# Kernel tuning notes

Hardware: AMD Instinct MI355X
Metric: run time of the kernel (lower is better)

The kernel has to match this reference:

```python
import jax, jax.numpy as jnp
import numpy as np

N, F, E, T = 50000, 128, 800000, 8


def setup_inputs() -> dict:
    key = jax.random.key(0)
    ks = jax.random.split(key, 10)
    s = 1.0 / np.sqrt(F)
    return {
        "x": jax.random.normal(ks[0], (N, F), jnp.float32),
        "edge_index": jax.random.randint(ks[1], (2, E), 0, N, jnp.int64),
        "edge_weight": jax.random.uniform(ks[2], (E,), jnp.float32),
        "W0": jax.random.normal(ks[3], (F, F), jnp.float32) * s,
        "Wih": jax.random.normal(ks[4], (3 * F, F), jnp.float32) * s,
        "Whh": jax.random.normal(ks[5], (3 * F, F), jnp.float32) * s,
        "bih": jax.random.normal(ks[6], (3 * F,), jnp.float32) * s,
        "bhh": jax.random.normal(ks[7], (3 * F,), jnp.float32) * s,
        "Wlin": jax.random.normal(ks[8], (T, F), jnp.float32) * s,
        "blin": jax.random.normal(ks[9], (T,), jnp.float32) * s,
    }


def _evolve_weight(W0, Wih, Whh, bih, bhh):
    # One GRU step with input = hidden = W0 (rows of weight matrix as batch).
    gi = W0 @ Wih.T + bih  # [F, 3F]
    gh = W0 @ Whh.T + bhh
    ir, iz, inn = jnp.split(gi, 3, axis=1)
    hr, hz, hn = jnp.split(gh, 3, axis=1)
    r = jax.nn.sigmoid(ir + hr)
    z = jax.nn.sigmoid(iz + hz)
    n = jnp.tanh(inn + r * hn)
    return (1.0 - z) * n + z * W0  # [F, F]


def reference(x, edge_index, edge_weight, W0, Wih, Whh, bih, bhh, Wlin, blin):
    n_nodes = x.shape[0]
    W = _evolve_weight(W0, Wih, Whh, bih, bhh)
    # gcn_norm with added self-loops (fill value 1.0), symmetric normalization
    loop = jnp.arange(n_nodes, dtype=edge_index.dtype)
    row = jnp.concatenate([edge_index[0], loop])
    col = jnp.concatenate([edge_index[1], loop])
    ew = jnp.concatenate([edge_weight, jnp.ones((n_nodes,), edge_weight.dtype)])
    deg = jax.ops.segment_sum(ew, col, num_segments=n_nodes)
    dinv = jnp.where(deg > 0, jax.lax.rsqrt(jnp.where(deg > 0, deg, 1.0)), 0.0)
    norm = dinv[row] * ew * dinv[col]  # [E+N]
    xw = x @ W  # [N, F]
    h = jax.ops.segment_sum(norm[:, None] * xw[row], col, num_segments=n_nodes)
    h = jax.nn.relu(h)
    return h @ Wlin.T + blin  # [N, n_target]
```

## Files before the change

kernel.cpp:

```cpp
#include <hip/hip_runtime.h>
#include <math.h>

#define F 128
#define FIX_SCALE 16777216.0f
#define FIX_INV   (1.0f / 16777216.0f)
#define CNT_SHIFT 40
#define DEG_MASK  ((1ULL << 40) - 1)

using bf16x8 = __attribute__((ext_vector_type(8))) short;
using f32x4  = __attribute__((ext_vector_type(4))) float;

__device__ inline int read_idx(const int* ei, long long elem, int i64) {
    return i64 ? (int)((const long long*)ei)[elem] : ei[elem];
}
__device__ inline unsigned int f2bf_rn(float f) {
    unsigned int b = __float_as_uint(f);
    return (b + 0x7FFFu + ((b >> 16) & 1u)) >> 16;
}
__device__ inline float bflo(unsigned int u) { return __uint_as_float(u << 16); }
__device__ inline float bfhi(unsigned int u) { return __uint_as_float(u & 0xFFFF0000u); }

__global__ void k_init(unsigned long long* packed, int* flag, const int* ei, int N) {
    int i = blockIdx.x * blockDim.x + threadIdx.x;
    if (i < N) packed[i] = 0ULL;
    if (i == 0) {
        int i64 = 1;
        for (int j = 0; j < 32; ++j) if (ei[2 * j + 1] != 0) { i64 = 0; break; }
        *flag = i64;
    }
}

__global__ void k_count(const int* ei, const float* ew, unsigned long long* packed,
                        int* pos, const int* flag, int E) {
    int e = blockIdx.x * blockDim.x + threadIdx.x;
    if (e >= E) return;
    int i64 = *flag;
    int c = read_idx(ei, (long long)E + e, i64);
    unsigned long long u = (1ULL << CNT_SHIFT) |
                           (unsigned long long)(ew[e] * FIX_SCALE + 0.5f);
    unsigned long long old = atomicAdd(&packed[c], u);
    pos[e] = (int)(old >> CNT_SHIFT);
}

__global__ void k_bsum(const unsigned long long* __restrict__ packed,
                       int* __restrict__ bsum, int N) {
    __shared__ int s[4];
    int i = blockIdx.x * 256 + threadIdx.x;
    int v = (i < N) ? (int)(packed[i] >> CNT_SHIFT) : 0;
    #pragma unroll
    for (int o = 1; o < 64; o <<= 1) v += __shfl_xor(v, o, 64);
    if ((threadIdx.x & 63) == 0) s[threadIdx.x >> 6] = v;
    __syncthreads();
    if (threadIdx.x == 0) bsum[blockIdx.x] = s[0] + s[1] + s[2] + s[3];
}

__global__ void k_bscan(int* bsum, int nb) {
    __shared__ int sdata[1024];
    int tid = threadIdx.x;
    int run = 0;
    for (int base = 0; base < nb; base += 1024) {
        int i = base + tid;
        int v = (i < nb) ? bsum[i] : 0;
        sdata[tid] = v;
        __syncthreads();
        #pragma unroll
        for (int s = 1; s < 1024; s <<= 1) {
            int add = (tid >= s) ? sdata[tid - s] : 0;
            __syncthreads();
            sdata[tid] += add;
            __syncthreads();
        }
        if (i < nb) bsum[i] = run + sdata[tid] - v;
        run += sdata[1023];
        __syncthreads();
    }
}

__global__ void k_offs(const unsigned long long* __restrict__ packed,
                       const int* __restrict__ bsum,
                       int* __restrict__ off, float* __restrict__ dinv, int N, int E) {
    __shared__ int sdata[256];
    int t = threadIdx.x;
    int i = blockIdx.x * 256 + t;
    unsigned long long p = (i < N) ? packed[i] : 0ULL;
    int v = (int)(p >> CNT_SHIFT);
    sdata[t] = v;
    __syncthreads();
    #pragma unroll
    for (int s = 1; s < 256; s <<= 1) {
        int add = (t >= s) ? sdata[t - s] : 0;
        __syncthreads();
        sdata[t] += add;
        __syncthreads();
    }
    if (i < N) {
        off[i] = bsum[blockIdx.x] + sdata[t] - v;
        float deg = 1.0f + (float)(p & DEG_MASK) * FIX_INV;
        dinv[i] = rsqrtf(deg);
        if (i == N - 1) off[N] = E;
    }
}

__global__ void k_place(const int* ei, const float* ew,
                        const int* __restrict__ off, const int* __restrict__ pos,
                        int2* ep, const int* flag, int E) {
    int e = blockIdx.x * blockDim.x + threadIdx.x;
    if (e >= E) return;
    int i64 = *flag;
    int r = read_idx(ei, e, i64);
    int c = read_idx(ei, (long long)E + e, i64);
    ep[off[c] + pos[e]] = make_int2(r, __float_as_int(ew[e]));
}

__global__ void k_evolve(const float* __restrict__ W0, const float* __restrict__ Wih,
                         const float* __restrict__ Whh, const float* __restrict__ bih,
                         const float* __restrict__ bhh,
                         unsigned short* __restrict__ Wth,
                         unsigned short* __restrict__ Wtl) {
    __shared__ __align__(16) float w0row[F];
    int i = blockIdx.x;
    int j = threadIdx.x;
    w0row[j] = W0[i * F + j];
    __syncthreads();
    float air = 0, aiz = 0, ain = 0, ahr = 0, ahz = 0, ahn = 0;
    const float* ir_p = Wih + (size_t)j * F;
    const float* iz_p = Wih + (size_t)(j + F) * F;
    const float* in_p = Wih + (size_t)(j + 2 * F) * F;
    const float* hr_p = Whh + (size_t)j * F;
    const float* hz_p = Whh + (size_t)(j + F) * F;
    const float* hn_p = Whh + (size_t)(j + 2 * F) * F;
    for (int k = 0; k < F; k += 4) {
        float4 w0 = *(const float4*)&w0row[k];
        float4 a;
        a = *(const float4*)&ir_p[k]; air += w0.x*a.x + w0.y*a.y + w0.z*a.z + w0.w*a.w;
        a = *(const float4*)&iz_p[k]; aiz += w0.x*a.x + w0.y*a.y + w0.z*a.z + w0.w*a.w;
        a = *(const float4*)&in_p[k]; ain += w0.x*a.x + w0.y*a.y + w0.z*a.z + w0.w*a.w;
        a = *(const float4*)&hr_p[k]; ahr += w0.x*a.x + w0.y*a.y + w0.z*a.z + w0.w*a.w;
        a = *(const float4*)&hz_p[k]; ahz += w0.x*a.x + w0.y*a.y + w0.z*a.z + w0.w*a.w;
        a = *(const float4*)&hn_p[k]; ahn += w0.x*a.x + w0.y*a.y + w0.z*a.z + w0.w*a.w;
    }
    air += bih[j];         ahr += bhh[j];
    aiz += bih[j + F];     ahz += bhh[j + F];
    ain += bih[j + 2*F];   ahn += bhh[j + 2*F];
    float r = 1.0f / (1.0f + expf(-(air + ahr)));
    float z = 1.0f / (1.0f + expf(-(aiz + ahz)));
    float n = tanhf(ain + r * ahn);
    float w = (1.0f - z) * n + z * w0row[j];
    unsigned int hb = f2bf_rn(w);
    float whi = __uint_as_float(hb << 16);
    unsigned int lb = f2bf_rn(w - whi);
    Wth[j * F + i] = (unsigned short)hb;
    Wtl[j * F + i] = (unsigned short)lb;
}

__global__ void k_cast(const float2* __restrict__ x2, const float* __restrict__ dinv,
                       unsigned int* __restrict__ xs, int M ) {
    int id = blockIdx.x * 256 + threadIdx.x;
    if (id >= M) return;
    float di = dinv[id >> 6];
    float2 v = x2[id];
    xs[id] = f2bf_rn(di * v.x) | (f2bf_rn(di * v.y) << 16);
}

__global__ __launch_bounds__(256) void k_agg2(const uint4* __restrict__ xs4,
                                              const int* __restrict__ off,
                                              const int2* __restrict__ ep,
                                              const float* __restrict__ dinv,
                                              uint4* __restrict__ hagg4, int N) {
    int wave = threadIdx.x >> 6, lane = threadIdx.x & 63;
    int c = blockIdx.x * 4 + wave;
    if (c >= N) return;
    int g = lane >> 4, sl = lane & 15;
    int start = off[c], end = off[c + 1];
    float a0[8] = {0,0,0,0,0,0,0,0}, a1[8] = {0,0,0,0,0,0,0,0};
    if (g == 0) {
        uint4 v = xs4[(size_t)c * 16 + sl];
        a0[0] = bflo(v.x); a0[1] = bfhi(v.x);
        a0[2] = bflo(v.y); a0[3] = bfhi(v.y);
        a0[4] = bflo(v.z); a0[5] = bfhi(v.z);
        a0[6] = bflo(v.w); a0[7] = bfhi(v.w);
    }
    for (int k = start; k < end; k += 8) {
        int iA = k + g, iB = k + g + 4;
        bool okA = iA < end, okB = iB < end;
        int2 eA, eB;
        if (okA) eA = ep[iA];
        if (okB) eB = ep[iB];
        if (okA) {
            uint4 v = xs4[(size_t)eA.x * 16 + sl];
            float w = __int_as_float(eA.y);
            a0[0] += w * bflo(v.x); a0[1] += w * bfhi(v.x);
            a0[2] += w * bflo(v.y); a0[3] += w * bfhi(v.y);
            a0[4] += w * bflo(v.z); a0[5] += w * bfhi(v.z);
            a0[6] += w * bflo(v.w); a0[7] += w * bfhi(v.w);
        }
        if (okB) {
            uint4 v = xs4[(size_t)eB.x * 16 + sl];
            float w = __int_as_float(eB.y);
            a1[0] += w * bflo(v.x); a1[1] += w * bfhi(v.x);
            a1[2] += w * bflo(v.y); a1[3] += w * bfhi(v.y);
            a1[4] += w * bflo(v.z); a1[5] += w * bfhi(v.z);
            a1[6] += w * bflo(v.w); a1[7] += w * bfhi(v.w);
        }
    }
    #pragma unroll
    for (int f = 0; f < 8; ++f) {
        float v = a0[f] + a1[f];
        v += __shfl_xor(v, 16, 64);
        v += __shfl_xor(v, 32, 64);
        a0[f] = v;
    }
    if (lane < 16) {
        float di = dinv[c];
        uint4 o;
        o.x = f2bf_rn(di * a0[0]) | (f2bf_rn(di * a0[1]) << 16);
        o.y = f2bf_rn(di * a0[2]) | (f2bf_rn(di * a0[3]) << 16);
        o.z = f2bf_rn(di * a0[4]) | (f2bf_rn(di * a0[5]) << 16);
        o.w = f2bf_rn(di * a0[6]) | (f2bf_rn(di * a0[7]) << 16);
        hagg4[(size_t)c * 16 + lane] = o;
    }
}

__global__ __launch_bounds__(256) void k_gemm(const uint4* __restrict__ hagg4,
                                              const unsigned short* __restrict__ Wth,
                                              const unsigned short* __restrict__ Wtl,
                                              const float* __restrict__ Wlin,
                                              const float* __restrict__ blin,
                                              float* __restrict__ out, int N) {
    __shared__ __align__(16) unsigned int At[64 * 68];
    __shared__ __align__(16) float WlinL[8 * F];
    int t = threadIdx.x;
    int row0 = blockIdx.x * 64;
    #pragma unroll
    for (int it = 0; it < 4; ++it) {
        int idx = it * 256 + t;
        int rr = idx >> 4, c4 = idx & 15;
        uint4 v = make_uint4(0u, 0u, 0u, 0u);
        if (row0 + rr < N) v = hagg4[(size_t)(row0 + rr) * 16 + c4];
        *(uint4*)&At[rr * 68 + c4 * 4] = v;
    }
    *(float4*)&WlinL[t * 4] = *(const float4*)&Wlin[t * 4];
    __syncthreads();

    int wave = t >> 6, lane = t & 63;
    int sl = lane & 15, q = lane >> 4;
    const unsigned short* Ash = (const unsigned short*)At;
    int mrow = wave * 16 + sl;

    f32x4 acc[8];
    #pragma unroll
    for (int nt = 0; nt < 8; ++nt) acc[nt] = (f32x4){0.f, 0.f, 0.f, 0.f};
    #pragma unroll
    for (int ko = 0; ko < 4; ++ko) {
        bf16x8 a = *(const bf16x8*)&Ash[mrow * 136 + ko * 32 + q * 8];
        #pragma unroll
        for (int nt = 0; nt < 8; ++nt) {
            int boff = (nt * 16 + sl) * F + ko * 32 + q * 8;
            bf16x8 bh = *(const bf16x8*)&Wth[boff];
            bf16x8 bl = *(const bf16x8*)&Wtl[boff];
            acc[nt] = __builtin_amdgcn_mfma_f32_16x16x32_bf16(a, bh, acc[nt], 0, 0, 0);
            acc[nt] = __builtin_amdgcn_mfma_f32_16x16x32_bf16(a, bl, acc[nt], 0, 0, 0);
        }
    }
    #pragma unroll
    for (int nt = 0; nt < 8; ++nt)
        #pragma unroll
        for (int r = 0; r < 4; ++r) acc[nt][r] = fmaxf(acc[nt][r], 0.f);

    float p[8][4];
    #pragma unroll
    for (int tt = 0; tt < 8; ++tt) {
        float wl[8];
        #pragma unroll
        for (int nt = 0; nt < 8; ++nt) wl[nt] = WlinL[tt * F + nt * 16 + sl];
        #pragma unroll
        for (int r = 0; r < 4; ++r) {
            float s = 0.f;
            #pragma unroll
            for (int nt = 0; nt < 8; ++nt) s += acc[nt][r] * wl[nt];
            p[tt][r] = s;
        }
    }
    #pragma unroll
    for (int tt = 0; tt < 8; ++tt)
        #pragma unroll
        for (int r = 0; r < 4; ++r) {
            float v = p[tt][r];
            v += __shfl_xor(v, 1, 64); v += __shfl_xor(v, 2, 64);
            v += __shfl_xor(v, 4, 64); v += __shfl_xor(v, 8, 64);
            p[tt][r] = v;
        }
    if (sl == 0) {
        #pragma unroll
        for (int r = 0; r < 4; ++r) {
            int row = row0 + wave * 16 + q * 4 + r;
            if (row < N) {
                #pragma unroll
                for (int tt = 0; tt < 8; ++tt)
                    out[(size_t)row * 8 + tt] = p[tt][r] + blin[tt];
            }
        }
    }
}

extern "C" void kernel_launch(void* const* d_in, const int* in_sizes, int n_in,
                              void* d_out, int out_size, void* d_ws, size_t ws_size,
                              hipStream_t stream) {
    const float* x    = (const float*)d_in[0];
    const int*   ei   = (const int*)d_in[1];
    const float* ew   = (const float*)d_in[2];
    const float* W0   = (const float*)d_in[3];
    const float* Wih  = (const float*)d_in[4];
    const float* Whh  = (const float*)d_in[5];
    const float* bih  = (const float*)d_in[6];
    const float* bhh  = (const float*)d_in[7];
    const float* Wlin = (const float*)d_in[8];
    const float* blin = (const float*)d_in[9];
    int N = in_sizes[0] / F;
    int E = in_sizes[1] / 2;
    float* outp = (float*)d_out;

    int nblk = (N + 255) / 256;

    char* wsb = (char*)d_ws;
    size_t cur = 0;
    auto alloc = [&](size_t sz) -> void* {
        void* p = wsb + cur;
        cur = (cur + sz + 255) & ~(size_t)255;
        return p;
    };
    unsigned long long* packed = (unsigned long long*)alloc((size_t)N * 8);
    float* dinv = (float*)alloc((size_t)N * 4);
    int*   off  = (int*)  alloc((size_t)(N + 1) * 4);
    int*   bsum = (int*)  alloc((size_t)nblk * 4);
    int*   flag = (int*)  alloc(256);
    int*   pos  = (int*)  alloc((size_t)E * 4);
    int2*  ep   = (int2*) alloc((size_t)E * 8);
    unsigned short* Wth = (unsigned short*)alloc((size_t)F * F * 2);
    unsigned short* Wtl = (unsigned short*)alloc((size_t)F * F * 2);
    unsigned int* xs    = (unsigned int*)alloc((size_t)N * 64 * 4);
    unsigned int* hagg  = (unsigned int*)alloc((size_t)N * 64 * 4);
    (void)ws_size; (void)n_in; (void)out_size;

    int M = N * 64;
    hipLaunchKernelGGL(k_init,   dim3(nblk),            dim3(256),  0, stream, packed, flag, ei, N);
    hipLaunchKernelGGL(k_count,  dim3((E + 255) / 256), dim3(256),  0, stream, ei, ew, packed, pos, flag, E);
    hipLaunchKernelGGL(k_bsum,   dim3(nblk),            dim3(256),  0, stream, packed, bsum, N);
    hipLaunchKernelGGL(k_bscan,  dim3(1),               dim3(1024), 0, stream, bsum, nblk);
    hipLaunchKernelGGL(k_offs,   dim3(nblk),            dim3(256),  0, stream, packed, bsum, off, dinv, N, E);
    hipLaunchKernelGGL(k_evolve, dim3(F),               dim3(F),    0, stream, W0, Wih, Whh, bih, bhh, Wth, Wtl);
    hipLaunchKernelGGL(k_place,  dim3((E + 255) / 256), dim3(256),  0, stream, ei, ew, off, pos, ep, flag, E);
    hipLaunchKernelGGL(k_cast,   dim3((M + 255) / 256), dim3(256),  0, stream, (const float2*)x, dinv, xs, M);
    hipLaunchKernelGGL(k_agg2,   dim3((N + 3) / 4),     dim3(256),  0, stream, (const uint4*)xs, off, ep, dinv, (uint4*)hagg, N);
    hipLaunchKernelGGL(k_gemm,   dim3((N + 63) / 64),   dim3(256),  0, stream, (const uint4*)hagg, Wth, Wtl, Wlin, blin, outp, N);
}
```

Before: 245.0 us.

## Fuse aggregation into GEMM, merge place/cast/evolve, pad atomic counters

Fuses the CSR neighbour aggregation into the MFMA GEMM kernel so aggregated rows go straight to shared memory, with no hagg round-trip through global memory. The place, cast and weight-evolve kernels are merged into one launch by splitting on block index. The single-block scan is replaced by each block summing its preceding block sums. Per-node atomic counters are padded to a stride of 8 to cut atomic contention on shared cache lines. The cost is fewer aggregation waves in flight per block (64 rows per block of 4 waves), a redundant per-block prefix reduction, and an 8x larger counter buffer to zero.

```diff
diff --git a/kernel.cpp b/kernel.cpp
--- a/kernel.cpp
+++ b/kernel.cpp
@@ -6,6 +6,7 @@
 #define FIX_INV   (1.0f / 16777216.0f)
 #define CNT_SHIFT 40
 #define DEG_MASK  ((1ULL << 40) - 1)
+#define PSTRIDE 8
 
 using bf16x8 = __attribute__((ext_vector_type(8))) short;
 using f32x4  = __attribute__((ext_vector_type(4))) float;
@@ -20,9 +21,9 @@
 __device__ inline float bflo(unsigned int u) { return __uint_as_float(u << 16); }
 __device__ inline float bfhi(unsigned int u) { return __uint_as_float(u & 0xFFFF0000u); }
 
-__global__ void k_init(unsigned long long* packed, int* flag, const int* ei, int N) {
+__global__ void k_init(unsigned long long* packed, int* flag, const int* ei, int M8) {
     int i = blockIdx.x * blockDim.x + threadIdx.x;
-    if (i < N) packed[i] = 0ULL;
+    if (i < M8) packed[i] = 0ULL;
     if (i == 0) {
         int i64 = 1;
         for (int j = 0; j < 32; ++j) if (ei[2 * j + 1] != 0) { i64 = 0; break; }
@@ -38,7 +39,7 @@
     int c = read_idx(ei, (long long)E + e, i64);
     unsigned long long u = (1ULL << CNT_SHIFT) |
                            (unsigned long long)(ew[e] * FIX_SCALE + 0.5f);
-    unsigned long long old = atomicAdd(&packed[c], u);
+    unsigned long long old = atomicAdd(&packed[(size_t)c * PSTRIDE], u);
     pos[e] = (int)(old >> CNT_SHIFT);
 }
 
@@ -46,7 +47,7 @@
                        int* __restrict__ bsum, int N) {
     __shared__ int s[4];
     int i = blockIdx.x * 256 + threadIdx.x;
-    int v = (i < N) ? (int)(packed[i] >> CNT_SHIFT) : 0;
+    int v = (i < N) ? (int)(packed[(size_t)i * PSTRIDE] >> CNT_SHIFT) : 0;
     #pragma unroll
     for (int o = 1; o < 64; o <<= 1) v += __shfl_xor(v, o, 64);
     if ((threadIdx.x & 63) == 0) s[threadIdx.x >> 6] = v;
@@ -54,35 +55,24 @@
     if (threadIdx.x == 0) bsum[blockIdx.x] = s[0] + s[1] + s[2] + s[3];
 }
 
-__global__ void k_bscan(int* bsum, int nb) {
-    __shared__ int sdata[1024];
-    int tid = threadIdx.x;
-    int run = 0;
-    for (int base = 0; base < nb; base += 1024) {
-        int i = base + tid;
-        int v = (i < nb) ? bsum[i] : 0;
-        sdata[tid] = v;
-        __syncthreads();
-        #pragma unroll
-        for (int s = 1; s < 1024; s <<= 1) {
-            int add = (tid >= s) ? sdata[tid - s] : 0;
-            __syncthreads();
-            sdata[tid] += add;
-            __syncthreads();
-        }
-        if (i < nb) bsum[i] = run + sdata[tid] - v;
-        run += sdata[1023];
-        __syncthreads();
-    }
-}
-
-__global__ void k_offs(const unsigned long long* __restrict__ packed,
-                       const int* __restrict__ bsum,
-                       int* __restrict__ off, float* __restrict__ dinv, int N, int E) {
+__global__ void k_offs2(const unsigned long long* __restrict__ packed,
+                        const int* __restrict__ bsum,
+                        int* __restrict__ off, float* __restrict__ dinv, int N, int E) {
+    __shared__ int sred[256];
     __shared__ int sdata[256];
     int t = threadIdx.x;
+    int pre = 0;
+    for (int j = t; j < blockIdx.x; j += 256) pre += bsum[j];
+    sred[t] = pre;
+    __syncthreads();
+    #pragma unroll
+    for (int s = 128; s > 0; s >>= 1) {
+        if (t < s) sred[t] += sred[t + s];
+        __syncthreads();
+    }
+    int base = sred[0];
     int i = blockIdx.x * 256 + t;
-    unsigned long long p = (i < N) ? packed[i] : 0ULL;
+    unsigned long long p = (i < N) ? packed[(size_t)i * PSTRIDE] : 0ULL;
     int v = (int)(p >> CNT_SHIFT);
     sdata[t] = v;
     __syncthreads();
@@ -94,33 +84,49 @@
         __syncthreads();
     }
     if (i < N) {
-        off[i] = bsum[blockIdx.x] + sdata[t] - v;
+        off[i] = base + sdata[t] - v;
         float deg = 1.0f + (float)(p & DEG_MASK) * FIX_INV;
         dinv[i] = rsqrtf(deg);
         if (i == N - 1) off[N] = E;
     }
 }
 
-__global__ void k_place(const int* ei, const float* ew,
-                        const int* __restrict__ off, const int* __restrict__ pos,
-                        int2* ep, const int* flag, int E) {
-    int e = blockIdx.x * blockDim.x + threadIdx.x;
-    if (e >= E) return;
-    int i64 = *flag;
-    int r = read_idx(ei, e, i64);
-    int c = read_idx(ei, (long long)E + e, i64);
-    ep[off[c] + pos[e]] = make_int2(r, __float_as_int(ew[e]));
-}
-
-__global__ void k_evolve(const float* __restrict__ W0, const float* __restrict__ Wih,
-                         const float* __restrict__ Whh, const float* __restrict__ bih,
-                         const float* __restrict__ bhh,
-                         unsigned short* __restrict__ Wth,
-                         unsigned short* __restrict__ Wtl) {
-    __shared__ __align__(16) float w0row[F];
-    int i = blockIdx.x;
-    int j = threadIdx.x;
-    w0row[j] = W0[i * F + j];
+__global__ __launch_bounds__(256) void k_pce(
+        const int* ei, const float* ew, const int* __restrict__ off,
+        const int* __restrict__ pos, int2* ep, const int* flag, int E, int nPlaceBlk,
+        const float2* __restrict__ x2, const float* __restrict__ dinv,
+        unsigned int* __restrict__ xs, int M, int nCastBlk,
+        const float* __restrict__ W0, const float* __restrict__ Wih,
+        const float* __restrict__ Whh, const float* __restrict__ bih,
+        const float* __restrict__ bhh,
+        unsigned short* __restrict__ Wth, unsigned short* __restrict__ Wtl) {
+    int b = blockIdx.x;
+    if (b < nPlaceBlk) {
+        int e = b * 256 + threadIdx.x;
+        if (e < E) {
+            int i64 = *flag;
+            int r = read_idx(ei, e, i64);
+            int c = read_idx(ei, (long long)E + e, i64);
+            ep[off[c] + pos[e]] = make_int2(r, __float_as_int(ew[e]));
+        }
+        return;
+    }
+    b -= nPlaceBlk;
+    if (b < nCastBlk) {
+        int id = b * 256 + threadIdx.x;
+        if (id < M) {
+            float di = dinv[id >> 6];
+            float2 v = x2[id];
+            xs[id] = f2bf_rn(di * v.x) | (f2bf_rn(di * v.y) << 16);
+        }
+        return;
+    }
+    b -= nCastBlk;
+    __shared__ __align__(16) float w0row[2][F];
+    int half = threadIdx.x >> 7;
+    int i = b * 2 + half;
+    int j = threadIdx.x & 127;
+    w0row[half][j] = W0[i * F + j];
     __syncthreads();
     float air = 0, aiz = 0, ain = 0, ahr = 0, ahz = 0, ahn = 0;
     const float* ir_p = Wih + (size_t)j * F;
@@ -130,7 +136,7 @@
     const float* hz_p = Whh + (size_t)(j + F) * F;
     const float* hn_p = Whh + (size_t)(j + 2 * F) * F;
     for (int k = 0; k < F; k += 4) {
-        float4 w0 = *(const float4*)&w0row[k];
+        float4 w0 = *(const float4*)&w0row[half][k];
         float4 a;
         a = *(const float4*)&ir_p[k]; air += w0.x*a.x + w0.y*a.y + w0.z*a.z + w0.w*a.w;
         a = *(const float4*)&iz_p[k]; aiz += w0.x*a.x + w0.y*a.y + w0.z*a.z + w0.w*a.w;
@@ -145,7 +151,7 @@
     float r = 1.0f / (1.0f + expf(-(air + ahr)));
     float z = 1.0f / (1.0f + expf(-(aiz + ahz)));
     float n = tanhf(ain + r * ahn);
-    float w = (1.0f - z) * n + z * w0row[j];
+    float w = (1.0f - z) * n + z * w0row[half][j];
     unsigned int hb = f2bf_rn(w);
     float whi = __uint_as_float(hb << 16);
     unsigned int lb = f2bf_rn(w - whi);
@@ -153,97 +159,81 @@
     Wtl[j * F + i] = (unsigned short)lb;
 }
 
-__global__ void k_cast(const float2* __restrict__ x2, const float* __restrict__ dinv,
-                       unsigned int* __restrict__ xs, int M ) {
-    int id = blockIdx.x * 256 + threadIdx.x;
-    if (id >= M) return;
-    float di = dinv[id >> 6];
-    float2 v = x2[id];
-    xs[id] = f2bf_rn(di * v.x) | (f2bf_rn(di * v.y) << 16);
-}
-
-__global__ __launch_bounds__(256) void k_agg2(const uint4* __restrict__ xs4,
-                                              const int* __restrict__ off,
-                                              const int2* __restrict__ ep,
-                                              const float* __restrict__ dinv,
-                                              uint4* __restrict__ hagg4, int N) {
-    int wave = threadIdx.x >> 6, lane = threadIdx.x & 63;
-    int c = blockIdx.x * 4 + wave;
-    if (c >= N) return;
-    int g = lane >> 4, sl = lane & 15;
-    int start = off[c], end = off[c + 1];
-    float a0[8] = {0,0,0,0,0,0,0,0}, a1[8] = {0,0,0,0,0,0,0,0};
-    if (g == 0) {
-        uint4 v = xs4[(size_t)c * 16 + sl];
-        a0[0] = bflo(v.x); a0[1] = bfhi(v.x);
-        a0[2] = bflo(v.y); a0[3] = bfhi(v.y);
-        a0[4] = bflo(v.z); a0[5] = bfhi(v.z);
-        a0[6] = bflo(v.w); a0[7] = bfhi(v.w);
-    }
-    for (int k = start; k < end; k += 8) {
-        int iA = k + g, iB = k + g + 4;
-        bool okA = iA < end, okB = iB < end;
-        int2 eA, eB;
-        if (okA) eA = ep[iA];
-        if (okB) eB = ep[iB];
-        if (okA) {
-            uint4 v = xs4[(size_t)eA.x * 16 + sl];
-            float w = __int_as_float(eA.y);
-            a0[0] += w * bflo(v.x); a0[1] += w * bfhi(v.x);
-            a0[2] += w * bflo(v.y); a0[3] += w * bfhi(v.y);
-            a0[4] += w * bflo(v.z); a0[5] += w * bfhi(v.z);
-            a0[6] += w * bflo(v.w); a0[7] += w * bfhi(v.w);
-        }
-        if (okB) {
-            uint4 v = xs4[(size_t)eB.x * 16 + sl];
-            float w = __int_as_float(eB.y);
-            a1[0] += w * bflo(v.x); a1[1] += w * bfhi(v.x);
-            a1[2] += w * bflo(v.y); a1[3] += w * bfhi(v.y);
-            a1[4] += w * bflo(v.z); a1[5] += w * bfhi(v.z);
-            a1[6] += w * bflo(v.w); a1[7] += w * bfhi(v.w);
-        }
-    }
-    #pragma unroll
-    for (int f = 0; f < 8; ++f) {
-        float v = a0[f] + a1[f];
-        v += __shfl_xor(v, 16, 64);
-        v += __shfl_xor(v, 32, 64);
-        a0[f] = v;
-    }
-    if (lane < 16) {
-        float di = dinv[c];
-        uint4 o;
-        o.x = f2bf_rn(di * a0[0]) | (f2bf_rn(di * a0[1]) << 16);
-        o.y = f2bf_rn(di * a0[2]) | (f2bf_rn(di * a0[3]) << 16);
-        o.z = f2bf_rn(di * a0[4]) | (f2bf_rn(di * a0[5]) << 16);
-        o.w = f2bf_rn(di * a0[6]) | (f2bf_rn(di * a0[7]) << 16);
-        hagg4[(size_t)c * 16 + lane] = o;
-    }
-}
-
-__global__ __launch_bounds__(256) void k_gemm(const uint4* __restrict__ hagg4,
-                                              const unsigned short* __restrict__ Wth,
-                                              const unsigned short* __restrict__ Wtl,
-                                              const float* __restrict__ Wlin,
-                                              const float* __restrict__ blin,
-                                              float* __restrict__ out, int N) {
+__global__ __launch_bounds__(256) void k_agg_gemm(const uint4* __restrict__ xs4,
+                                                  const int* __restrict__ off,
+                                                  const int2* __restrict__ ep,
+                                                  const float* __restrict__ dinv,
+                                                  const unsigned short* __restrict__ Wth,
+                                                  const unsigned short* __restrict__ Wtl,
+                                                  const float* __restrict__ Wlin,
+                                                  const float* __restrict__ blin,
+                                                  float* __restrict__ out, int N) {
     __shared__ __align__(16) unsigned int At[64 * 68];
     __shared__ __align__(16) float WlinL[8 * F];
-    int t = threadIdx.x;
+    int t = threadIdx.x, wave = t >> 6, lane = t & 63;
     int row0 = blockIdx.x * 64;
-    #pragma unroll
-    for (int it = 0; it < 4; ++it) {
-        int idx = it * 256 + t;
-        int rr = idx >> 4, c4 = idx & 15;
-        uint4 v = make_uint4(0u, 0u, 0u, 0u);
-        if (row0 + rr < N) v = hagg4[(size_t)(row0 + rr) * 16 + c4];
-        *(uint4*)&At[rr * 68 + c4 * 4] = v;
-    }
     *(float4*)&WlinL[t * 4] = *(const float4*)&Wlin[t * 4];
-    __syncthreads();
-
-    int wave = t >> 6, lane = t & 63;
-    int sl = lane & 15, q = lane >> 4;
+
+    int g = lane >> 4, sl = lane & 15;
+    for (int i = 0; i < 16; ++i) {
+        int rr = wave * 16 + i;
+        int c = row0 + rr;
+        if (c < N) {
+            int start = off[c], end = off[c + 1];
+            float a0[8] = {0,0,0,0,0,0,0,0}, a1[8] = {0,0,0,0,0,0,0,0};
+            if (g == 0) {
+                uint4 v = xs4[(size_t)c * 16 + sl];
+                a0[0] = bflo(v.x); a0[1] = bfhi(v.x);
+                a0[2] = bflo(v.y); a0[3] = bfhi(v.y);
+                a0[4] = bflo(v.z); a0[5] = bfhi(v.z);
+                a0[6] = bflo(v.w); a0[7] = bfhi(v.w);
+            }
+            for (int k = start; k < end; k += 8) {
+                int iA = k + g, iB = k + g + 4;
+                bool okA = iA < end, okB = iB < end;
+                int2 eA, eB;
+                if (okA) eA = ep[iA];
+                if (okB) eB = ep[iB];
+                if (okA) {
+                    uint4 v = xs4[(size_t)eA.x * 16 + sl];
+                    float w = __int_as_float(eA.y);
+                    a0[0] += w * bflo(v.x); a0[1] += w * bfhi(v.x);
+                    a0[2] += w * bflo(v.y); a0[3] += w * bfhi(v.y);
+                    a0[4] += w * bflo(v.z); a0[5] += w * bfhi(v.z);
+                    a0[6] += w * bflo(v.w); a0[7] += w * bfhi(v.w);
+                }
+                if (okB) {
+                    uint4 v = xs4[(size_t)eB.x * 16 + sl];
+                    float w = __int_as_float(eB.y);
+                    a1[0] += w * bflo(v.x); a1[1] += w * bfhi(v.x);
+                    a1[2] += w * bflo(v.y); a1[3] += w * bfhi(v.y);
+                    a1[4] += w * bflo(v.z); a1[5] += w * bfhi(v.z);
+                    a1[6] += w * bflo(v.w); a1[7] += w * bfhi(v.w);
+                }
+            }
+            #pragma unroll
+            for (int f = 0; f < 8; ++f) {
+                float v = a0[f] + a1[f];
+                v += __shfl_xor(v, 16, 64);
+                v += __shfl_xor(v, 32, 64);
+                a0[f] = v;
+            }
+            if (g == 0) {
+                float di = dinv[c];
+                uint4 o;
+                o.x = f2bf_rn(di * a0[0]) | (f2bf_rn(di * a0[1]) << 16);
+                o.y = f2bf_rn(di * a0[2]) | (f2bf_rn(di * a0[3]) << 16);
+                o.z = f2bf_rn(di * a0[4]) | (f2bf_rn(di * a0[5]) << 16);
+                o.w = f2bf_rn(di * a0[6]) | (f2bf_rn(di * a0[7]) << 16);
+                *(uint4*)&At[rr * 68 + sl * 4] = o;
+            }
+        } else if (g == 0) {
+            *(uint4*)&At[rr * 68 + sl * 4] = make_uint4(0u, 0u, 0u, 0u);
+        }
+    }
+    __syncthreads();
+
+    int q = lane >> 4;
     const unsigned short* Ash = (const unsigned short*)At;
     int mrow = wave * 16 + sl;
 
@@ -329,7 +319,7 @@
         cur = (cur + sz + 255) & ~(size_t)255;
         return p;
     };
-    unsigned long long* packed = (unsigned long long*)alloc((size_t)N * 8);
+    unsigned long long* packed = (unsigned long long*)alloc((size_t)N * PSTRIDE * 8);
     float* dinv = (float*)alloc((size_t)N * 4);
     int*   off  = (int*)  alloc((size_t)(N + 1) * 4);
     int*   bsum = (int*)  alloc((size_t)nblk * 4);
@@ -339,18 +329,22 @@
     unsigned short* Wth = (unsigned short*)alloc((size_t)F * F * 2);
     unsigned short* Wtl = (unsigned short*)alloc((size_t)F * F * 2);
     unsigned int* xs    = (unsigned int*)alloc((size_t)N * 64 * 4);
-    unsigned int* hagg  = (unsigned int*)alloc((size_t)N * 64 * 4);
     (void)ws_size; (void)n_in; (void)out_size;
 
-    int M = N * 64;
-    hipLaunchKernelGGL(k_init,   dim3(nblk),            dim3(256),  0, stream, packed, flag, ei, N);
-    hipLaunchKernelGGL(k_count,  dim3((E + 255) / 256), dim3(256),  0, stream, ei, ew, packed, pos, flag, E);
-    hipLaunchKernelGGL(k_bsum,   dim3(nblk),            dim3(256),  0, stream, packed, bsum, N);
-    hipLaunchKernelGGL(k_bscan,  dim3(1),               dim3(1024), 0, stream, bsum, nblk);
-    hipLaunchKernelGGL(k_offs,   dim3(nblk),            dim3(256),  0, stream, packed, bsum, off, dinv, N, E);
-    hipLaunchKernelGGL(k_evolve, dim3(F),               dim3(F),    0, stream, W0, Wih, Whh, bih, bhh, Wth, Wtl);
-    hipLaunchKernelGGL(k_place,  dim3((E + 255) / 256), dim3(256),  0, stream, ei, ew, off, pos, ep, flag, E);
-    hipLaunchKernelGGL(k_cast,   dim3((M + 255) / 256), dim3(256),  0, stream, (const float2*)x, dinv, xs, M);
-    hipLaunchKernelGGL(k_agg2,   dim3((N + 3) / 4),     dim3(256),  0, stream, (const uint4*)xs, off, ep, dinv, (uint4*)hagg, N);
-    hipLaunchKernelGGL(k_gemm,   dim3((N + 63) / 64),   dim3(256),  0, stream, (const uint4*)hagg, Wth, Wtl, Wlin, blin, outp, N);
-}
+    int M  = N * 64;
+    int M8 = N * PSTRIDE;
+    int nPlaceBlk = (E + 255) / 256;
+    int nCastBlk  = (M + 255) / 256;
+    int nEvolveBlk = F / 2;
+
+    hipLaunchKernelGGL(k_init,  dim3((M8 + 255) / 256), dim3(256), 0, stream, packed, flag, ei, M8);
+    hipLaunchKernelGGL(k_count, dim3(nPlaceBlk),        dim3(256), 0, stream, ei, ew, packed, pos, flag, E);
+    hipLaunchKernelGGL(k_bsum,  dim3(nblk),             dim3(256), 0, stream, packed, bsum, N);
+    hipLaunchKernelGGL(k_offs2, dim3(nblk),             dim3(256), 0, stream, packed, bsum, off, dinv, N, E);
+    hipLaunchKernelGGL(k_pce,   dim3(nPlaceBlk + nCastBlk + nEvolveBlk), dim3(256), 0, stream,
+                       ei, ew, off, pos, ep, flag, E, nPlaceBlk,
+                       (const float2*)x, dinv, xs, M, nCastBlk,
+                       W0, Wih, Whh, bih, bhh, Wth, Wtl);
+    hipLaunchKernelGGL(k_agg_gemm, dim3((N + 63) / 64), dim3(256), 0, stream,
+                       (const uint4*)xs, off, ep, dinv, Wth, Wtl, Wlin, blin, outp, N);
+}
```

After: 281.6 us. 1.15x slower.
